# Optimization experiments

Hardware: AMD Instinct MI355X
Metric: run time of the kernel (lower is better)

The kernel has to match this reference:

```python
import jax, jax.numpy as jnp
import numpy as np

B, C, H, W = 8, 256, 48, 48

def setup_inputs() -> dict:
    key = jax.random.key(0)
    ks = jax.random.split(key, 8)
    s = 1.0 / np.sqrt(C)  # conv2d default init scale (uniform fan_in)
    x = jax.random.normal(ks[0], (B, C, H, W), dtype=jnp.float32)
    y = jax.random.normal(ks[1], (B, C, H, W), dtype=jnp.float32)
    Wq = jax.random.uniform(ks[2], (C, C), jnp.float32, -s, s)
    bq = jax.random.uniform(ks[3], (C,), jnp.float32, -s, s)
    Wk = jax.random.uniform(ks[4], (C, C), jnp.float32, -s, s)
    bk = jax.random.uniform(ks[5], (C,), jnp.float32, -s, s)
    Wv = jax.random.uniform(ks[6], (C, C), jnp.float32, -s, s)
    bv = jax.random.uniform(ks[7], (C,), jnp.float32, -s, s)
    return {"x": x, "y": y, "Wq": Wq, "bq": bq, "Wk": Wk, "bk": bk, "Wv": Wv, "bv": bv}

def reference(x, y, Wq, bq, Wk, bk, Wv, bv):
    b, c, h, w = x.shape
    n = h * w
    # [B,C,H,W] -> tokens [B,N,C]
    xt = x.reshape(b, c, n).transpose(0, 2, 1)
    yt = y.reshape(b, c, n).transpose(0, 2, 1)
    # 1x1 convs == per-token linear projections
    q = xt @ Wq.T + bq  # [B,N,C]
    k = yt @ Wk.T + bk  # [B,N,C]
    v = yt @ Wv.T + bv  # [B,N,C]
    # unscaled QK^T softmax (module applies no 1/sqrt(d) scaling)
    scores = jnp.einsum('bnc,bmc->bnm', q, k)  # [B,N,N]
    attn = jax.nn.softmax(scores, axis=-1)
    out = jnp.einsum('bnm,bmc->bnc', attn, v)  # [B,N,C]
    return out.transpose(0, 2, 1).reshape(b, c, h, w)
```

## Files before the change

kernel.cpp:

```cpp
#include <hip/hip_runtime.h>
#include <stdint.h>

#define Bb 8
#define Cc 256
#define Nn 2304
#define PJT 18
#define QT 18
#define KSPLIT 3
#define TPS 24
#define L2E 1.44269504088896f
#define DEFER_THR 8.0f

#define AS1 __attribute__((address_space(1)))
#define AS3 __attribute__((address_space(3)))

typedef unsigned short u16;
typedef unsigned int u32;
typedef _Float16 h16;
typedef h16  h16x8 __attribute__((ext_vector_type(8)));
typedef u16  u16x8 __attribute__((ext_vector_type(8)));
typedef u16  u16x4 __attribute__((ext_vector_type(4)));
typedef u32  u32x4 __attribute__((ext_vector_type(4)));
typedef float f32x4 __attribute__((ext_vector_type(4)));
typedef float f32x2 __attribute__((ext_vector_type(2)));

static __device__ __forceinline__ u16 f2h(float f) {
  return __builtin_bit_cast(u16, (h16)f);
}
static __device__ __forceinline__ float h2f(u16 v) {
  return (float)__builtin_bit_cast(h16, v);
}
static __device__ __forceinline__ h16x8 ash(u16x8 v) {
  return __builtin_bit_cast(h16x8, v);
}
static __device__ __forceinline__ f32x4 mfma16(u16x8 a, u16x8 b, f32x4 c) {
  return __builtin_amdgcn_mfma_f32_16x16x32_f16(ash(a), ash(b), c, 0, 0, 0);
}
static __device__ __forceinline__ u32 pkf16(float a, float b) {
  return __builtin_bit_cast(u32, __builtin_amdgcn_cvt_pkrtz(a, b));
}

__global__ void prep_kernel(const float* __restrict__ Wq,
                            const float* __restrict__ Wk,
                            const float* __restrict__ Wv,
                            u16* __restrict__ Wf)
{
  const int tid = blockIdx.x * 256 + threadIdx.x;
  const int m   = tid >> 13;
  const int off = (tid & 8191) * 8;
  const float* src = (m == 0) ? Wq : (m == 1) ? Wk : Wv;
  const f32x4 a = *(const f32x4*)(src + off);
  const f32x4 c = *(const f32x4*)(src + off + 4);
  u16x8 o;
#pragma unroll
  for (int j = 0; j < 4; ++j) { o[j] = f2h(a[j]); o[j + 4] = f2h(c[j]); }
  *(u16x8*)(Wf + (size_t)m * 65536 + off) = o;
}

__global__ __launch_bounds__(256, 2) void proj_kernel(
    const float* __restrict__ x, const float* __restrict__ y,
    const u16* __restrict__ Wf,
    const float* __restrict__ bq, const float* __restrict__ bk,
    const float* __restrict__ bv,
    u16* __restrict__ Qf, u16* __restrict__ Kf, u16* __restrict__ Vf)
{
  __shared__ u16 sW[2][32 * 256];
  const int t    = threadIdx.x;
  const int b    = blockIdx.x;
  const int q0   = blockIdx.y * 128;
  const int z    = blockIdx.z;
  const int lane = t & 63;
  const int w    = t >> 6;
  const int quad = lane >> 4;
  const int l15  = lane & 15;

  const u16* WZ = Wf + (size_t)z * 65536;

  const int rbase = 2 * w + (lane >> 5);
  const int wcol  = ((lane & 31) ^ rbase) << 3;

  auto stage = [&](int rg, int buf) {
#pragma unroll
    for (int it = 0; it < 4; ++it) {
      __builtin_amdgcn_global_load_lds(
          (const AS1 void*)(WZ + (size_t)(rg * 32 + rbase + 8 * it) * 256 + wcol),
          (AS3 void*)&sW[buf][(w + 4 * it) * 512], 16, 0, 0);
    }
  };

  stage(0, 0);

  const float* src = (z == 0) ? x : y;
  u16x8 af[2][8];
#pragma unroll
  for (int g = 0; g < 2; ++g) {
    const int tok = q0 + g * 64 + w * 16 + l15;
#pragma unroll
    for (int kc = 0; kc < 8; ++kc) {
      const float* p = src + ((size_t)b * Cc + kc * 32 + quad * 8) * Nn + tok;
      float v[8];
#pragma unroll
      for (int j = 0; j < 8; ++j) v[j] = p[(size_t)j * Nn];
#pragma unroll
      for (int j = 0; j < 8; ++j) af[g][kc][j] = f2h(v[j]);
    }
  }

  f32x4 acc[2][16];
#pragma unroll
  for (int g = 0; g < 2; ++g)
#pragma unroll
    for (int i = 0; i < 16; ++i) acc[g][i] = (f32x4){0.f, 0.f, 0.f, 0.f};

  int cur = 0;
#pragma unroll 1
  for (int rg = 0; rg < 8; ++rg) {
    __builtin_amdgcn_s_waitcnt(0x0F70);
    __syncthreads();
    if (rg + 1 < 8) stage(rg + 1, cur ^ 1);
#pragma unroll
    for (int cbl = 0; cbl < 2; ++cbl) {
      const int rl = cbl * 16 + l15;
      f32x4 a0 = acc[0][rg * 2 + cbl];
      f32x4 a1 = acc[1][rg * 2 + cbl];
#pragma unroll
      for (int kc = 0; kc < 8; ++kc) {
        const u16x8 bf = *(const u16x8*)(sW[cur] + rl * 256 + (((kc * 4 + quad) ^ (rl & 7)) << 3));
        if (z < 2) {
          a0 = mfma16(af[0][kc], bf, a0);
          a1 = mfma16(af[1][kc], bf, a1);
        } else {
          a0 = mfma16(bf, af[0][kc], a0);
          a1 = mfma16(bf, af[1][kc], a1);
        }
      }
      acc[0][rg * 2 + cbl] = a0;
      acc[1][rg * 2 + cbl] = a1;
    }
    cur ^= 1;
  }

  if (z < 2) {
    const float* bias = (z == 0) ? bq : bk;
    u16* O = (z == 0) ? Qf : Kf;
#pragma unroll
    for (int g = 0; g < 2; ++g) {
#pragma unroll
      for (int cb = 0; cb < 16; ++cb) {
        const int co = cb * 16 + l15;
        const float bs = bias[co];
        const size_t base = ((size_t)b * Nn + q0 + g * 64 + w * 16 + quad * 4) * Cc + co;
#pragma unroll
        for (int r = 0; r < 4; ++r)
          O[base + (size_t)r * Cc] = f2h(acc[g][cb][r] + bs);
      }
    }
  } else {
#pragma unroll
    for (int g = 0; g < 2; ++g) {
#pragma unroll
      for (int cb = 0; cb < 16; ++cb) {
        const int crow = cb * 16 + quad * 4;
#pragma unroll
        for (int r = 0; r < 4; ++r)
          Vf[((size_t)b * Cc + crow + r) * Nn + q0 + g * 64 + w * 16 + l15] =
              f2h(acc[g][cb][r] + bv[crow + r]);
      }
    }
  }
}

__global__ __launch_bounds__(256, 2) void attn_kernel(
    const u16* __restrict__ Qf, const u16* __restrict__ Kf,
    const u16* __restrict__ Vf, u16* __restrict__ OpH,
    float* __restrict__ Ml)
{
  __shared__ u16 sK[2][32 * 256];
  __shared__ u16 sV[2][256 * 32];
  const int t    = threadIdx.x;
  const int b    = blockIdx.x;
  const int q0   = blockIdx.y * 128;
  const int sp   = blockIdx.z;
  const int lane = t & 63;
  const int w    = t >> 6;
  const int quad = lane >> 4;
  const int l15  = lane & 15;
  const int wq0  = q0 + w * 32;

  const u16* Kb = Kf + (size_t)b * Nn * Cc;
  const u16* Vb = Vf + (size_t)b * Cc * Nn;

  const int rbase = 2 * w + (lane >> 5);
  const int kcol  = ((lane & 31) ^ rbase) << 3;
  const int rb2 = rbase >> 2, rb3 = rbase & 3;
  int koff[4];
#pragma unroll
  for (int it = 0; it < 4; ++it) {
    const int key = (((rb2 + 2 * it) & 3) << 3) + rb3 + ((it >> 1) << 2);
    koff[it] = key * Cc + kcol;
  }
  const u16* Kt = Kb + (size_t)(sp * TPS * 32) * Cc;
  const int cV   = w * 16 + (lane >> 2);
  const int vcol = ((lane & 3) ^ ((cV >> 1) & 3)) << 3;
  const u16* vp0 = Vb + (size_t)cV * Nn + sp * TPS * 32 + vcol;

  auto stage = [&](int kb, int buf) {
#pragma unroll
    for (int it = 0; it < 4; ++it) {
      __builtin_amdgcn_global_load_lds(
          (const AS1 void*)(Kt + (size_t)kb * 32 * Cc + koff[it]),
          (AS3 void*)&sK[buf][(w + 4 * it) * 512], 16, 0, 0);
      __builtin_amdgcn_global_load_lds(
          (const AS1 void*)(vp0 + kb * 32 + (size_t)it * 64 * Nn),
          (AS3 void*)&sV[buf][(w + 4 * it) * 512], 16, 0, 0);
    }
  };

  stage(0, 0);

  u16x8 qf[2][8];
#pragma unroll
  for (int g = 0; g < 2; ++g) {
    const size_t qrow = ((size_t)b * Nn + wq0 + g * 16 + l15) * Cc;
#pragma unroll
    for (int kc = 0; kc < 8; ++kc)
      qf[g][kc] = *(const u16x8*)(Qf + qrow + kc * 32 + quad * 8);
  }

  f32x4 o[2][16];
#pragma unroll
  for (int g = 0; g < 2; ++g)
#pragma unroll
    for (int i = 0; i < 16; ++i) o[g][i] = (f32x4){0.f, 0.f, 0.f, 0.f};
  float mrow[2] = {-3e38f, -3e38f};
  float lrow[2] = {0.f, 0.f};

  const int vbase = l15 * 32 + ((quad ^ ((l15 >> 1) & 3)) << 3);

  int cur = 0;
#pragma unroll 1
  for (int kb = 0; kb < TPS; ++kb) {
    __builtin_amdgcn_s_waitcnt(0x0F70);
    __syncthreads();
    if (kb + 1 < TPS) stage(kb + 1, cur ^ 1);

    f32x4 s[2][2];
    s[0][0] = (f32x4){0.f, 0.f, 0.f, 0.f}; s[0][1] = s[0][0];
    s[1][0] = s[0][0];                      s[1][1] = s[0][0];
#pragma unroll
    for (int kc = 0; kc < 8; ++kc) {
      const int ch = ((kc * 4 + quad) ^ (l15 & 7)) << 3;
      const u16x8 k0 = *(const u16x8*)(sK[cur] + l15 * 256 + ch);
      const u16x8 k1 = *(const u16x8*)(sK[cur] + (16 + l15) * 256 + ch);
      s[0][0] = mfma16(k0, qf[0][kc], s[0][0]);
      s[0][1] = mfma16(k1, qf[0][kc], s[0][1]);
      s[1][0] = mfma16(k0, qf[1][kc], s[1][0]);
      s[1][1] = mfma16(k1, qf[1][kc], s[1][1]);
    }

    u16x8 pf[2];
    float al[2];
    int needany = 0;
#pragma unroll
    for (int g = 0; g < 2; ++g) {
      float mloc = fmaxf(
          fmaxf(fmaxf(s[g][0][0], s[g][0][1]), fmaxf(s[g][0][2], s[g][0][3])),
          fmaxf(fmaxf(s[g][1][0], s[g][1][1]), fmaxf(s[g][1][2], s[g][1][3])));
      mloc = fmaxf(mloc, __shfl_xor(mloc, 16, 64));
      mloc = fmaxf(mloc, __shfl_xor(mloc, 32, 64));
      const bool need = mloc > mrow[g] + DEFER_THR;
      const float mn  = need ? mloc : mrow[g];
      al[g] = need ? exp2f((mrow[g] - mn) * L2E) : 1.f;
      mrow[g] = mn;
      needany |= (int)need;

      float p[8];
      float sum = 0.f;
#pragma unroll
      for (int r = 0; r < 4; ++r) {
        p[r]     = exp2f((s[g][0][r] - mn) * L2E);
        p[4 + r] = exp2f((s[g][1][r] - mn) * L2E);
        sum += p[r] + p[4 + r];
      }
      sum += __shfl_xor(sum, 16, 64);
      sum += __shfl_xor(sum, 32, 64);
      lrow[g] = lrow[g] * al[g] + sum;

      u32x4 pw;
      pw[0] = pkf16(p[0], p[1]);
      pw[1] = pkf16(p[2], p[3]);
      pw[2] = pkf16(p[4], p[5]);
      pw[3] = pkf16(p[6], p[7]);
      pf[g] = __builtin_bit_cast(u16x8, pw);
    }

    if (__any(needany)) {
#pragma unroll
      for (int i = 0; i < 16; ++i) {
#pragma unroll
        for (int r = 0; r < 4; ++r) {
          o[0][i][r] *= al[0];
          o[1][i][r] *= al[1];
        }
      }
    }

#pragma unroll
    for (int cb = 0; cb < 16; ++cb) {
      const u16x8 vf = *(const u16x8*)(sV[cur] + cb * 512 + vbase);
      o[0][cb] = mfma16(vf, pf[0], o[0][cb]);
      o[1][cb] = mfma16(vf, pf[1], o[1][cb]);
    }

    cur ^= 1;
  }

  u16* Ob = OpH + ((size_t)sp * Bb + b) * (size_t)Cc * Nn;
#pragma unroll
  for (int g = 0; g < 2; ++g) {
    const float inv = 1.f / lrow[g];
    const int qn = wq0 + g * 16 + l15;
#pragma unroll
    for (int cb = 0; cb < 16; ++cb) {
#pragma unroll
      for (int r = 0; r < 4; ++r)
        Ob[(size_t)(cb * 16 + quad * 4 + r) * Nn + qn] = f2h(o[g][cb][r] * inv);
    }
  }
  if (lane < 16) {
    float* mlb = Ml + ((size_t)sp * Bb + b) * (size_t)Nn * 2;
#pragma unroll
    for (int g = 0; g < 2; ++g) {
      const int qn = wq0 + g * 16 + l15;
      *(f32x2*)(mlb + (size_t)qn * 2) = (f32x2){mrow[g], lrow[g]};
    }
  }
}

__global__ void merge_kernel(const u16* __restrict__ OpH,
                             const float* __restrict__ Ml,
                             float* __restrict__ out)
{
  const int idx = blockIdx.x * 256 + threadIdx.x;
  const int n4 = idx % 576;
  const int bc = idx / 576;
  const int b  = bc >> 8;
  const size_t obase = (size_t)bc * Nn + n4 * 4;

  float oh[KSPLIT][4], mv[KSPLIT][4], lv[KSPLIT][4];
#pragma unroll
  for (int s = 0; s < KSPLIT; ++s) {
    const u16x4 hv = *(const u16x4*)(OpH + ((size_t)s * Bb * Cc + bc) * Nn + n4 * 4);
#pragma unroll
    for (int j = 0; j < 4; ++j) oh[s][j] = h2f(hv[j]);
    const float* ml = Ml + ((size_t)s * Bb + b) * (size_t)Nn * 2 + n4 * 8;
    const f32x4 u0 = *(const f32x4*)ml;
    const f32x4 u1 = *(const f32x4*)(ml + 4);
#pragma unroll
    for (int j = 0; j < 4; ++j) {
      mv[s][j] = (j < 2) ? u0[j * 2]     : u1[(j - 2) * 2];
      lv[s][j] = (j < 2) ? u0[j * 2 + 1] : u1[(j - 2) * 2 + 1];
    }
  }

  f32x4 r;
#pragma unroll
  for (int j = 0; j < 4; ++j) {
    float m = mv[0][j];
#pragma unroll
    for (int s = 1; s < KSPLIT; ++s) m = fmaxf(m, mv[s][j]);
    float num = 0.f, den = 0.f;
#pragma unroll
    for (int s = 0; s < KSPLIT; ++s) {
      const float ws = lv[s][j] * exp2f((mv[s][j] - m) * L2E);
      num += oh[s][j] * ws;
      den += ws;
    }
    r[j] = num / den;
  }
  *(f32x4*)(out + obase) = r;
}

extern "C" void kernel_launch(void* const* d_in, const int* in_sizes, int n_in,
                              void* d_out, int out_size, void* d_ws, size_t ws_size,
                              hipStream_t stream) {
  const float* x  = (const float*)d_in[0];
  const float* y  = (const float*)d_in[1];
  const float* Wq = (const float*)d_in[2];
  const float* bq = (const float*)d_in[3];
  const float* Wk = (const float*)d_in[4];
  const float* bk = (const float*)d_in[5];
  const float* Wv = (const float*)d_in[6];
  const float* bv = (const float*)d_in[7];
  float* out = (float*)d_out;

  const size_t NC = (size_t)Bb * Nn * Cc;
  u16* Qf = (u16*)d_ws;
  u16* Kf = Qf + NC;
  u16* Vf = Kf + NC;
  u16* Wf = Vf + NC;
  u16* OpH = Wf + 3 * 65536;
  float* Ml = (float*)(OpH + (size_t)KSPLIT * NC);

  hipLaunchKernelGGL(prep_kernel, dim3(96), dim3(256), 0, stream,
                     Wq, Wk, Wv, Wf);
  hipLaunchKernelGGL(proj_kernel, dim3(Bb, PJT, 3), dim3(256), 0, stream,
                     x, y, Wf, bq, bk, bv, Qf, Kf, Vf);
  hipLaunchKernelGGL(attn_kernel, dim3(Bb, QT, KSPLIT), dim3(256), 0, stream,
                     Qf, Kf, Vf, OpH, Ml);
  hipLaunchKernelGGL(merge_kernel, dim3(4608), dim3(256), 0, stream,
                     OpH, Ml, out);
}
```

Measured before the change: 227.9 us.

## Stage projection outputs through LDS for coalesced stores; interleave softmax with PV MFMAs

The projection kernel now writes its results into a swizzled LDS tile and then emits 16-byte coalesced global stores for Q/K rows and V columns, instead of scattered 2-byte stores. In the attention kernel, the softmax for the second query group is split out and placed after the first group's PV MFMAs, so exp work can overlap with matrix ops. s_setprio is raised around MFMA blocks to favour those waves. This adds extra barriers and LDS traffic in the projection epilogue, and the split loop may increase register pressure.

```diff
diff --git a/kernel.cpp b/kernel.cpp
--- a/kernel.cpp
+++ b/kernel.cpp
@@ -140,31 +140,53 @@
     cur ^= 1;
   }
 
+  u16* sT = &sW[0][0];
   if (z < 2) {
     const float* bias = (z == 0) ? bq : bk;
     u16* O = (z == 0) ? Qf : Kf;
 #pragma unroll
     for (int g = 0; g < 2; ++g) {
+      __syncthreads();
 #pragma unroll
       for (int cb = 0; cb < 16; ++cb) {
-        const int co = cb * 16 + l15;
-        const float bs = bias[co];
-        const size_t base = ((size_t)b * Nn + q0 + g * 64 + w * 16 + quad * 4) * Cc + co;
-#pragma unroll
-        for (int r = 0; r < 4; ++r)
-          O[base + (size_t)r * Cc] = f2h(acc[g][cb][r] + bs);
+        const int col = cb * 16 + l15;
+        const float bs = bias[col];
+#pragma unroll
+        for (int r = 0; r < 4; ++r) {
+          const int row = w * 16 + quad * 4 + r;
+          sT[row * 256 + (col ^ ((row & 7) << 3))] = f2h(acc[g][cb][r] + bs);
+        }
+      }
+      __syncthreads();
+      const size_t ob = ((size_t)b * Nn + q0 + g * 64) * Cc;
+#pragma unroll
+      for (int i = 0; i < 8; ++i) {
+        const int lin = i * 256 + t;
+        const int row = lin >> 5, ch = lin & 31;
+        const u16x8 v = *(const u16x8*)(sT + row * 256 + ((ch ^ (row & 7)) << 3));
+        *(u16x8*)(O + ob + (size_t)lin * 8) = v;
       }
     }
   } else {
 #pragma unroll
     for (int g = 0; g < 2; ++g) {
+      __syncthreads();
 #pragma unroll
       for (int cb = 0; cb < 16; ++cb) {
-        const int crow = cb * 16 + quad * 4;
-#pragma unroll
-        for (int r = 0; r < 4; ++r)
-          Vf[((size_t)b * Cc + crow + r) * Nn + q0 + g * 64 + w * 16 + l15] =
-              f2h(acc[g][cb][r] + bv[crow + r]);
+#pragma unroll
+        for (int r = 0; r < 4; ++r) {
+          const int c = cb * 16 + quad * 4 + r;
+          const int col = w * 16 + l15;
+          sT[c * 64 + (col ^ ((c & 7) << 3))] = f2h(acc[g][cb][r] + bv[c]);
+        }
+      }
+      __syncthreads();
+#pragma unroll
+      for (int i = 0; i < 8; ++i) {
+        const int lin = i * 256 + t;
+        const int row = lin >> 3, g8 = lin & 7;
+        const u16x8 v = *(const u16x8*)(sT + row * 64 + ((g8 ^ (row & 7)) << 3));
+        *(u16x8*)(Vf + ((size_t)b * Cc + row) * Nn + q0 + g * 64 + g8 * 8) = v;
       }
     }
   }
@@ -247,6 +269,7 @@
     f32x4 s[2][2];
     s[0][0] = (f32x4){0.f, 0.f, 0.f, 0.f}; s[0][1] = s[0][0];
     s[1][0] = s[0][0];                      s[1][1] = s[0][0];
+    __builtin_amdgcn_s_setprio(1);
 #pragma unroll
     for (int kc = 0; kc < 8; ++kc) {
       const int ch = ((kc * 4 + quad) ^ (l15 & 7)) << 3;
@@ -257,60 +280,89 @@
       s[1][0] = mfma16(k0, qf[1][kc], s[1][0]);
       s[1][1] = mfma16(k1, qf[1][kc], s[1][1]);
     }
-
-    u16x8 pf[2];
-    float al[2];
-    int needany = 0;
-#pragma unroll
-    for (int g = 0; g < 2; ++g) {
+    __builtin_amdgcn_s_setprio(0);
+
+    u16x8 pf0, pf1;
+    float al0, al1;
+    bool need0, need1;
+    {
       float mloc = fmaxf(
-          fmaxf(fmaxf(s[g][0][0], s[g][0][1]), fmaxf(s[g][0][2], s[g][0][3])),
-          fmaxf(fmaxf(s[g][1][0], s[g][1][1]), fmaxf(s[g][1][2], s[g][1][3])));
+          fmaxf(fmaxf(s[0][0][0], s[0][0][1]), fmaxf(s[0][0][2], s[0][0][3])),
+          fmaxf(fmaxf(s[0][1][0], s[0][1][1]), fmaxf(s[0][1][2], s[0][1][3])));
       mloc = fmaxf(mloc, __shfl_xor(mloc, 16, 64));
       mloc = fmaxf(mloc, __shfl_xor(mloc, 32, 64));
-      const bool need = mloc > mrow[g] + DEFER_THR;
-      const float mn  = need ? mloc : mrow[g];
-      al[g] = need ? exp2f((mrow[g] - mn) * L2E) : 1.f;
-      mrow[g] = mn;
-      needany |= (int)need;
-
-      float p[8];
-      float sum = 0.f;
+      need0 = mloc > mrow[0] + DEFER_THR;
+      const float mn = need0 ? mloc : mrow[0];
+      al0 = need0 ? exp2f((mrow[0] - mn) * L2E) : 1.f;
+      mrow[0] = mn;
+      float p[8], sum = 0.f;
 #pragma unroll
       for (int r = 0; r < 4; ++r) {
-        p[r]     = exp2f((s[g][0][r] - mn) * L2E);
-        p[4 + r] = exp2f((s[g][1][r] - mn) * L2E);
+        p[r]     = exp2f((s[0][0][r] - mn) * L2E);
+        p[4 + r] = exp2f((s[0][1][r] - mn) * L2E);
         sum += p[r] + p[4 + r];
       }
       sum += __shfl_xor(sum, 16, 64);
       sum += __shfl_xor(sum, 32, 64);
-      lrow[g] = lrow[g] * al[g] + sum;
-
+      lrow[0] = lrow[0] * al0 + sum;
       u32x4 pw;
-      pw[0] = pkf16(p[0], p[1]);
-      pw[1] = pkf16(p[2], p[3]);
-      pw[2] = pkf16(p[4], p[5]);
-      pw[3] = pkf16(p[6], p[7]);
-      pf[g] = __builtin_bit_cast(u16x8, pw);
-    }
-
-    if (__any(needany)) {
-#pragma unroll
-      for (int i = 0; i < 16; ++i) {
-#pragma unroll
-        for (int r = 0; r < 4; ++r) {
-          o[0][i][r] *= al[0];
-          o[1][i][r] *= al[1];
-        }
-      }
-    }
-
+      pw[0] = pkf16(p[0], p[1]); pw[1] = pkf16(p[2], p[3]);
+      pw[2] = pkf16(p[4], p[5]); pw[3] = pkf16(p[6], p[7]);
+      pf0 = __builtin_bit_cast(u16x8, pw);
+    }
+    if (__any(need0)) {
+#pragma unroll
+      for (int i = 0; i < 16; ++i)
+#pragma unroll
+        for (int r = 0; r < 4; ++r) o[0][i][r] *= al0;
+    }
+
+    __builtin_amdgcn_s_setprio(1);
 #pragma unroll
     for (int cb = 0; cb < 16; ++cb) {
       const u16x8 vf = *(const u16x8*)(sV[cur] + cb * 512 + vbase);
-      o[0][cb] = mfma16(vf, pf[0], o[0][cb]);
-      o[1][cb] = mfma16(vf, pf[1], o[1][cb]);
-    }
+      o[0][cb] = mfma16(vf, pf0, o[0][cb]);
+    }
+    __builtin_amdgcn_s_setprio(0);
+    {
+      float mloc = fmaxf(
+          fmaxf(fmaxf(s[1][0][0], s[1][0][1]), fmaxf(s[1][0][2], s[1][0][3])),
+          fmaxf(fmaxf(s[1][1][0], s[1][1][1]), fmaxf(s[1][1][2], s[1][1][3])));
+      mloc = fmaxf(mloc, __shfl_xor(mloc, 16, 64));
+      mloc = fmaxf(mloc, __shfl_xor(mloc, 32, 64));
+      need1 = mloc > mrow[1] + DEFER_THR;
+      const float mn = need1 ? mloc : mrow[1];
+      al1 = need1 ? exp2f((mrow[1] - mn) * L2E) : 1.f;
+      mrow[1] = mn;
+      float p[8], sum = 0.f;
+#pragma unroll
+      for (int r = 0; r < 4; ++r) {
+        p[r]     = exp2f((s[1][0][r] - mn) * L2E);
+        p[4 + r] = exp2f((s[1][1][r] - mn) * L2E);
+        sum += p[r] + p[4 + r];
+      }
+      sum += __shfl_xor(sum, 16, 64);
+      sum += __shfl_xor(sum, 32, 64);
+      lrow[1] = lrow[1] * al1 + sum;
+      u32x4 pw;
+      pw[0] = pkf16(p[0], p[1]); pw[1] = pkf16(p[2], p[3]);
+      pw[2] = pkf16(p[4], p[5]); pw[3] = pkf16(p[6], p[7]);
+      pf1 = __builtin_bit_cast(u16x8, pw);
+    }
+    if (__any(need1)) {
+#pragma unroll
+      for (int i = 0; i < 16; ++i)
+#pragma unroll
+        for (int r = 0; r < 4; ++r) o[1][i][r] *= al1;
+    }
+
+    __builtin_amdgcn_s_setprio(1);
+#pragma unroll
+    for (int cb = 0; cb < 16; ++cb) {
+      const u16x8 vf = *(const u16x8*)(sV[cur] + cb * 512 + vbase);
+      o[1][cb] = mfma16(vf, pf1, o[1][cb]);
+    }
+    __builtin_amdgcn_s_setprio(0);
 
     cur ^= 1;
   }
```

Result: slower. 247.3 us (+8.5%).
